# Performance work log

Measured on AMD Instinct MI355X. Metric: run time of the kernel, lower is better.

## Reference

```python
import jax, jax.numpy as jnp
import numpy as np

EMBED_DIM = 512
NUM_HEADS = 8
HEAD_DIM = EMBED_DIM // NUM_HEADS


def setup_inputs() -> dict:
    key = jax.random.key(0)
    ks = jax.random.split(key, 5)
    B, N, D = 2, 4096, EMBED_DIM
    s_in = 1.0 / np.sqrt(D)
    x = jax.random.normal(ks[0], (B, N, D), dtype=jnp.float32)
    qkv_w = jax.random.uniform(ks[1], (3 * D, D), dtype=jnp.float32, minval=-s_in, maxval=s_in)
    qkv_b = jax.random.uniform(ks[2], (3 * D,), dtype=jnp.float32, minval=-s_in, maxval=s_in)
    out_w = jax.random.uniform(ks[3], (D, D), dtype=jnp.float32, minval=-s_in, maxval=s_in)
    out_b = jax.random.uniform(ks[4], (D,), dtype=jnp.float32, minval=-s_in, maxval=s_in)
    return {"x": x, "qkv_w": qkv_w, "qkv_b": qkv_b, "out_w": out_w, "out_b": out_b}


def reference(x, qkv_w, qkv_b, out_w, out_b):
    B, N, D = x.shape
    H, Hd = NUM_HEADS, HEAD_DIM
    # qkv projection: [B,N,3D] -> [3,B,H,N,Hd]
    qkv = x @ qkv_w.T + qkv_b
    qkv = qkv.reshape(B, N, 3, H, Hd).transpose(2, 0, 3, 1, 4)
    q, k, v = qkv[0], qkv[1], qkv[2]
    scale = 1.0 / jnp.sqrt(jnp.asarray(Hd, dtype=x.dtype))
    scores = jnp.einsum("bhnd,bhmd->bhnm", q, k) * scale  # [B,H,N,N]
    weights = jax.nn.softmax(scores, axis=-1)
    out = jnp.einsum("bhnm,bhmd->bhnd", weights, v)  # [B,H,N,Hd]
    out = out.transpose(0, 2, 1, 3).reshape(B, N, D)
    return out @ out_w.T + out_b
```

## Files before the change

kernel.cpp:

```cpp
#include <hip/hip_runtime.h>

typedef __attribute__((ext_vector_type(8))) short short8;
typedef __attribute__((ext_vector_type(2))) float f32x2;
typedef __attribute__((ext_vector_type(4))) float f32x4;
typedef __attribute__((ext_vector_type(16))) float f32x16;
typedef unsigned short u16;
typedef unsigned int u32;

#define SCQ 0.18033688011112042f

__device__ __forceinline__ u16 f2b(float f) {
  unsigned u = __builtin_bit_cast(unsigned, f);
  u += 0x7FFFu + ((u >> 16) & 1u);
  return (u16)(u >> 16);
}

__device__ __forceinline__ u32 cvtpk(float a, float b) {
  u32 r;
  asm("v_cvt_pk_bf16_f32 %0, %1, %2" : "=v"(r) : "v"(a), "v"(b));
  return r;
}

__device__ __forceinline__ float ex2(float x) { return __builtin_amdgcn_exp2f(x); }

__device__ __forceinline__ void gl_lds16(const u16* g, u16* l) {
  __builtin_amdgcn_global_load_lds(
      (const __attribute__((address_space(1))) unsigned int*)g,
      (__attribute__((address_space(3))) unsigned int*)l, 16, 0, 0);
}

__global__ __launch_bounds__(256) void convert_k(
    const float* __restrict__ x, const float* __restrict__ w1, const float* __restrict__ w2,
    u16* __restrict__ xb, u16* __restrict__ w1b, u16* __restrict__ w2b) {
  const int NXv = (8192 * 512) / 4;
  const int NW1v = (1536 * 512) / 4;
  const int NW2v = (512 * 512) / 4;
  int i = blockIdx.x * 256 + threadIdx.x;
  const float4* src;
  u16* dst;
  int j;
  float scale = 1.0f;
  if (i < NXv) {
    src = (const float4*)x; dst = xb; j = i;
  } else if (i < NXv + NW1v) {
    j = i - NXv; src = (const float4*)w1; dst = w1b;
    if (j < (512 * 512) / 4) scale = SCQ;
  } else {
    j = i - NXv - NW1v;
    if (j >= NW2v) return;
    src = (const float4*)w2; dst = w2b;
  }
  float4 v = src[j];
  ushort4 o;
  o.x = f2b(v.x * scale); o.y = f2b(v.y * scale);
  o.z = f2b(v.z * scale); o.w = f2b(v.w * scale);
  *reinterpret_cast<ushort4*>(dst + (size_t)j * 4) = o;
}

__global__ __launch_bounds__(256) void qkv_gemm(
    const u16* __restrict__ Ab, const u16* __restrict__ Bw, const float* __restrict__ bias,
    u16* __restrict__ Qd, u16* __restrict__ Kd, u16* __restrict__ Vtd) {
  const int m0 = blockIdx.x * 128, n0 = blockIdx.y * 128;
  const int tid = threadIdx.x, wave = tid >> 6, lane = tid & 63;
  const int g = lane >> 4, lr = lane & 15;
  const int wm = (wave >> 1) * 64, wn = (wave & 1) * 64;
  __shared__ alignas(16) u16 smem[32768];

  f32x4 acc[4][4];
#pragma unroll
  for (int mf = 0; mf < 4; ++mf)
#pragma unroll
    for (int nf = 0; nf < 4; ++nf)
#pragma unroll
      for (int r = 0; r < 4; ++r) acc[mf][nf][r] = 0.0f;

  const int gid0 = wave * 64 + lane;

#define QKV_STAGE(buf, k0)                                                         \
  {                                                                                \
    u16* Ad_ = smem + (buf) * 8192;                                                \
    u16* Bd_ = smem + 16384 + (buf) * 8192;                                        \
    _Pragma("unroll")                                                              \
    for (int c = 0; c < 4; ++c) {                                                  \
      const int gid = c * 256 + gid0;                                              \
      const int row = gid >> 3;                                                    \
      const int col = ((gid & 7) ^ (row & 7)) << 3;                                \
      gl_lds16(Ab + (size_t)(m0 + row) * 512 + (k0) + col,                         \
               Ad_ + (size_t)(c * 256 + wave * 64) * 8);                           \
      gl_lds16(Bw + (size_t)(n0 + row) * 512 + (k0) + col,                         \
               Bd_ + (size_t)(c * 256 + wave * 64) * 8);                           \
    }                                                                              \
  }

  QKV_STAGE(0, 0);
  __syncthreads();

#pragma unroll 1
  for (int kt = 0; kt < 8; ++kt) {
    const int cur = kt & 1;
    if (kt + 1 < 8) QKV_STAGE(cur ^ 1, (kt + 1) * 64);

    const u16* Ac = smem + cur * 8192;
    const u16* Bc = smem + 16384 + cur * 8192;
#pragma unroll
    for (int kb = 0; kb < 2; ++kb) {
      short8 bf[4], af[4];
#pragma unroll
      for (int nf = 0; nf < 4; ++nf)
        bf[nf] = *reinterpret_cast<const short8*>(
            &Bc[(wn + nf * 16 + lr) * 64 + (((kb * 4 + g) ^ (lr & 7)) << 3)]);
#pragma unroll
      for (int mf = 0; mf < 4; ++mf)
        af[mf] = *reinterpret_cast<const short8*>(
            &Ac[(wm + mf * 16 + lr) * 64 + (((kb * 4 + g) ^ (lr & 7)) << 3)]);
#pragma unroll
      for (int mf = 0; mf < 4; ++mf)
#pragma unroll
        for (int nf = 0; nf < 4; ++nf)
          acc[mf][nf] = __builtin_amdgcn_mfma_f32_16x16x32_bf16(af[mf], bf[nf], acc[mf][nf], 0, 0, 0);
    }
    __syncthreads();
  }
#undef QKV_STAGE

  u16* Ct = smem;
  const int b = m0 >> 12;
  const int which = n0 >> 9;
  const int nloc = m0 & 4095;

  if (which < 2) {
#pragma unroll
    for (int mf = 0; mf < 4; ++mf)
#pragma unroll
      for (int nf = 0; nf < 4; ++nf) {
        const int col_l = wn + nf * 16 + lr;
        float bv = bias[n0 + col_l];
        if (which == 0) bv *= SCQ;
#pragma unroll
        for (int r = 0; r < 4; ++r)
          Ct[(wm + mf * 16 + g * 4 + r) * 136 + col_l] = f2b(acc[mf][nf][r] + bv);
      }
    __syncthreads();
    u16* const dst0 = (which == 0) ? Qd : Kd;
#pragma unroll
    for (int p = 0; p < 8; ++p) {
      const int idx = p * 256 + tid;
      const int row = idx >> 4;
      const int c8 = (idx & 15) << 3;
      short8 v = *reinterpret_cast<const short8*>(&Ct[row * 136 + c8]);
      const int col = n0 + c8;
      const int h = (col & 511) >> 6, hd = col & 63;
      *reinterpret_cast<short8*>(
          dst0 + ((size_t)(b * 8 + h) * 4096 + nloc + row) * 64 + hd) = v;
    }
  } else {
#pragma unroll
    for (int mf = 0; mf < 4; ++mf)
#pragma unroll
      for (int nf = 0; nf < 4; ++nf) {
        const int col_l = wn + nf * 16 + lr;
        const float bv = bias[n0 + col_l];
        const int row0 = wm + mf * 16 + g * 4;
        ushort4 pk;
        pk.x = f2b(acc[mf][nf][0] + bv);
        pk.y = f2b(acc[mf][nf][1] + bv);
        pk.z = f2b(acc[mf][nf][2] + bv);
        pk.w = f2b(acc[mf][nf][3] + bv);
        *reinterpret_cast<ushort4*>(&Ct[col_l * 136 + row0]) = pk;
      }
    __syncthreads();
#pragma unroll
    for (int p = 0; p < 8; ++p) {
      const int idx = p * 256 + tid;
      const int col_l = idx >> 4;
      const int c8 = (idx & 15) << 3;
      short8 v = *reinterpret_cast<const short8*>(&Ct[col_l * 136 + c8]);
      const int col = n0 + col_l;
      const int h = (col & 511) >> 6, hd = col & 63;
      *reinterpret_cast<short8*>(
          Vtd + ((size_t)(b * 8 + h) * 64 + hd) * 4096 + nloc + c8) = v;
    }
  }
}

__global__ __launch_bounds__(256, 2) void attn13(
    const u16* __restrict__ Qd, const u16* __restrict__ Kd, const u16* __restrict__ Vtd,
    float* __restrict__ Op, float* __restrict__ Lp) {
  int f = blockIdx.x;
  int xcd = f & 7, slot = f >> 3;
  int bh = (xcd << 1) + (slot >> 5);
  int rem = slot & 31;
  int half = rem >> 4;
  int qb = rem & 15;

  const int tid = threadIdx.x, wave = tid >> 6, lane = tid & 63;
  const int hi = lane >> 5, lq = lane & 31;

  const u16* Qh = Qd + (size_t)bh * (4096 * 64);
  const u16* Kh = Kd + (size_t)bh * (4096 * 64);
  const u16* Vh = Vtd + (size_t)bh * (64 * 4096);
  float* Oh = Op + (size_t)half * (8192 * 512);
  float* Lh = Lp + (size_t)half * (16 * 4096);

  __shared__ alignas(16) u16 Kl[2][128 * 64];

  const int qrow_base = qb * 256 + wave * 64;

  short8 qf[2][4];
#pragma unroll
  for (int qt = 0; qt < 2; ++qt)
#pragma unroll
    for (int s = 0; s < 4; ++s)
      qf[qt][s] = *reinterpret_cast<const short8*>(
          Qh + (size_t)(qrow_base + qt * 32 + lq) * 64 + s * 16 + hi * 8);

  f32x16 acc[2][2];
#pragma unroll
  for (int qt = 0; qt < 2; ++qt)
#pragma unroll
    for (int dt = 0; dt < 2; ++dt)
#pragma unroll
      for (int i = 0; i < 16; ++i) acc[qt][dt][i] = 0.0f;

  f32x16 Z;
#pragma unroll
  for (int i = 0; i < 16; ++i) Z[i] = 0.0f;

  float lrun[2] = {0.0f, 0.0f};

  const int kv0 = half * 2048;
  const int gid0 = wave * 64 + lane;

#pragma unroll
  for (int c = 0; c < 4; ++c) {
    const int gid = c * 256 + gid0;
    const int row = gid >> 3;
    const int col = ((gid & 7) ^ (row & 7)) << 3;
    gl_lds16(Kh + (size_t)(kv0 + row) * 64 + col, &Kl[0][(c * 256 + wave * 64) * 8]);
  }
  __syncthreads();

  f32x16 stA0, stA1, stB0, stB1;
  short8 vfA[2][2], vfB[2][2];
  short8 pbA0[2], pbA1[2], pbB0[2], pbB1[2];

#define QK_HALF(st0, st1, h)                                                        \
  {                                                                                 \
    const int rb = ((h) * 32 + lq) * 64;                                            \
    __builtin_amdgcn_s_setprio(1);                                                  \
    _Pragma("unroll")                                                               \
    for (int s = 0; s < 4; ++s) {                                                   \
      const int ch = ((2 * s + hi) ^ (lq & 7)) << 3;                                \
      short8 kf = *reinterpret_cast<const short8*>(&Kl[cur][rb + ch]);              \
      if (s == 0) {                                                                 \
        st0 = __builtin_amdgcn_mfma_f32_32x32x16_bf16(kf, qf[0][0], Z, 0, 0, 0);    \
        st1 = __builtin_amdgcn_mfma_f32_32x32x16_bf16(kf, qf[1][0], Z, 0, 0, 0);    \
      } else {                                                                      \
        st0 = __builtin_amdgcn_mfma_f32_32x32x16_bf16(kf, qf[0][s], st0, 0, 0, 0);  \
        st1 = __builtin_amdgcn_mfma_f32_32x32x16_bf16(kf, qf[1][s], st1, 0, 0, 0);  \
      }                                                                             \
    }                                                                               \
    __builtin_amdgcn_s_setprio(0);                                                  \
  }

#define LOADV_HALF(vf, h)                                                           \
  {                                                                                 \
    const int off = kbase + (h) * 32 + hi * 8;                                      \
    vf[0][0] = *reinterpret_cast<const short8*>(Vh + (size_t)lq * 4096 + off);      \
    vf[0][1] = *reinterpret_cast<const short8*>(Vh + (size_t)(32 + lq) * 4096 + off); \
    vf[1][0] = *reinterpret_cast<const short8*>(Vh + (size_t)lq * 4096 + off + 16); \
    vf[1][1] = *reinterpret_cast<const short8*>(Vh + (size_t)(32 + lq) * 4096 + off + 16); \
  }

#define SM_QT(stq, pbq, qt_idx)                                                     \
  {                                                                                 \
    f32x2 p2[8];                                                                    \
    _Pragma("unroll")                                                               \
    for (int j = 0; j < 8; ++j) {                                                   \
      p2[j][0] = ex2(stq[2 * j]);                                                   \
      p2[j][1] = ex2(stq[2 * j + 1]);                                               \
    }                                                                               \
    f32x2 s0 = (p2[0] + p2[1]) + (p2[2] + p2[3]);                                   \
    f32x2 s1 = (p2[4] + p2[5]) + (p2[6] + p2[7]);                                   \
    f32x2 sm = s0 + s1;                                                             \
    lrun[qt_idx] += sm[0] + sm[1];                                                  \
    _Pragma("unroll")                                                               \
    for (int t = 0; t < 2; ++t) {                                                   \
      u32 wa = cvtpk(p2[4 * t + 0][0], p2[4 * t + 0][1]);                           \
      u32 wb = cvtpk(p2[4 * t + 2][0], p2[4 * t + 2][1]);                           \
      u32 wc = cvtpk(p2[4 * t + 1][0], p2[4 * t + 1][1]);                           \
      u32 wd = cvtpk(p2[4 * t + 3][0], p2[4 * t + 3][1]);                           \
      asm volatile("v_permlane32_swap_b32 %0, %1" : "+v"(wa), "+v"(wb));            \
      asm volatile("v_permlane32_swap_b32 %0, %1" : "+v"(wc), "+v"(wd));            \
      int4 wv;                                                                      \
      wv.x = (int)wa; wv.y = (int)wc; wv.z = (int)wb; wv.w = (int)wd;               \
      pbq[t] = __builtin_bit_cast(short8, wv);                                      \
    }                                                                               \
  }

#define PV_HALF(vf, pb0, pb1)                                                       \
  {                                                                                 \
    __builtin_amdgcn_s_setprio(1);                                                  \
    _Pragma("unroll")                                                               \
    for (int t = 0; t < 2; ++t) {                                                   \
      acc[0][0] = __builtin_amdgcn_mfma_f32_32x32x16_bf16(vf[t][0], pb0[t], acc[0][0], 0, 0, 0); \
      acc[0][1] = __builtin_amdgcn_mfma_f32_32x32x16_bf16(vf[t][1], pb0[t], acc[0][1], 0, 0, 0); \
      acc[1][0] = __builtin_amdgcn_mfma_f32_32x32x16_bf16(vf[t][0], pb1[t], acc[1][0], 0, 0, 0); \
      acc[1][1] = __builtin_amdgcn_mfma_f32_32x32x16_bf16(vf[t][1], pb1[t], acc[1][1], 0, 0, 0); \
    }                                                                               \
    __builtin_amdgcn_s_setprio(0);                                                  \
  }

#pragma unroll 1
  for (int kt = 0; kt < 16; ++kt) {
    const int cur = kt & 1;
    const int kbase = kv0 + kt * 128;

    if (kt + 1 < 16) {
      const u16* kn = Kh + (size_t)(kbase + 128) * 64;
#pragma unroll
      for (int c = 0; c < 4; ++c) {
        const int gid = c * 256 + gid0;
        const int row = gid >> 3;
        const int col = ((gid & 7) ^ (row & 7)) << 3;
        gl_lds16(kn + (size_t)row * 64 + col, &Kl[cur ^ 1][(c * 256 + wave * 64) * 8]);
      }
    }

    QK_HALF(stA0, stA1, 0);
    LOADV_HALF(vfA, 0);
#pragma unroll
    for (int hp = 0; hp < 2; ++hp) {
      const int h = hp * 2;
      QK_HALF(stB0, stB1, h + 1);
      LOADV_HALF(vfB, h + 1);
      SM_QT(stA0, pbA0, 0);
      SM_QT(stA1, pbA1, 1);
      PV_HALF(vfA, pbA0, pbA1);
      if (hp == 0) {
        QK_HALF(stA0, stA1, h + 2);
        LOADV_HALF(vfA, h + 2);
      }
      SM_QT(stB0, pbB0, 0);
      SM_QT(stB1, pbB1, 1);
      PV_HALF(vfB, pbB0, pbB1);
    }

    __syncthreads();
  }
#undef QK_HALF
#undef LOADV_HALF
#undef SM_QT
#undef PV_HALF

  const int b = bh >> 3, h = bh & 7;
#pragma unroll
  for (int qt = 0; qt < 2; ++qt) {
    const int qn = qrow_base + qt * 32 + lq;
    const size_t rowoff = ((size_t)(b * 4096 + qn)) * 512 + h * 64;
#pragma unroll
    for (int dt = 0; dt < 2; ++dt)
#pragma unroll
      for (int t = 0; t < 4; ++t) {
        f32x4 v4;
        v4[0] = acc[qt][dt][4 * t + 0];
        v4[1] = acc[qt][dt][4 * t + 1];
        v4[2] = acc[qt][dt][4 * t + 2];
        v4[3] = acc[qt][dt][4 * t + 3];
        *reinterpret_cast<f32x4*>(Oh + rowoff + dt * 32 + t * 8 + hi * 4) = v4;
      }
    float lt = lrun[qt] + __shfl_xor(lrun[qt], 32);
    if (hi == 0) Lh[(bh << 12) + qn] = lt;
  }
}

__global__ __launch_bounds__(256) void combine_k(
    const float* __restrict__ Op, const float* __restrict__ Lp,
    u16* __restrict__ attnb) {
  int idx = blockIdx.x * 256 + threadIdx.x;
  int row = idx >> 7, c4 = idx & 127;
  int b = row >> 12, n = row & 4095, h = c4 >> 4;
  int li = (((b << 3) + h) << 12) + n;
  float l = Lp[li] + Lp[li + 65536];
  float inv = 1.0f / l;
  const int STRIDE = 8192 * 512 / 4;
  float4 o0 = reinterpret_cast<const float4*>(Op)[idx];
  float4 o1 = reinterpret_cast<const float4*>(Op)[idx + STRIDE];
  ushort4 o;
  o.x = f2b((o0.x + o1.x) * inv);
  o.y = f2b((o0.y + o1.y) * inv);
  o.z = f2b((o0.z + o1.z) * inv);
  o.w = f2b((o0.w + o1.w) * inv);
  *reinterpret_cast<ushort4*>(attnb + (size_t)idx * 4) = o;
}

__global__ __launch_bounds__(256) void out_gemm(
    const u16* __restrict__ Ab, const u16* __restrict__ Bw, const float* __restrict__ bias,
    float* __restrict__ out) {
  const int m0 = blockIdx.x * 128, n0 = blockIdx.y * 128;
  const int tid = threadIdx.x, wave = tid >> 6, lane = tid & 63;
  const int g = lane >> 4, lr = lane & 15;
  const int wm = (wave >> 1) * 64, wn = (wave & 1) * 64;
  __shared__ alignas(16) u16 smem[32768];

  f32x4 acc[4][4];
#pragma unroll
  for (int mf = 0; mf < 4; ++mf)
#pragma unroll
    for (int nf = 0; nf < 4; ++nf)
#pragma unroll
      for (int r = 0; r < 4; ++r) acc[mf][nf][r] = 0.0f;

  const int gid0 = wave * 64 + lane;

#define OUT_STAGE(buf, k0)                                                         \
  {                                                                                \
    u16* Ad_ = smem + (buf) * 8192;                                                \
    u16* Bd_ = smem + 16384 + (buf) * 8192;                                        \
    _Pragma("unroll")                                                              \
    for (int c = 0; c < 4; ++c) {                                                  \
      const int gid = c * 256 + gid0;                                              \
      const int row = gid >> 3;                                                    \
      const int col = ((gid & 7) ^ (row & 7)) << 3;                                \
      gl_lds16(Ab + (size_t)(m0 + row) * 512 + (k0) + col,                         \
               Ad_ + (size_t)(c * 256 + wave * 64) * 8);                           \
      gl_lds16(Bw + (size_t)(n0 + row) * 512 + (k0) + col,                         \
               Bd_ + (size_t)(c * 256 + wave * 64) * 8);                           \
    }                                                                              \
  }

  OUT_STAGE(0, 0);
  __syncthreads();

#pragma unroll 1
  for (int kt = 0; kt < 8; ++kt) {
    const int cur = kt & 1;
    if (kt + 1 < 8) OUT_STAGE(cur ^ 1, (kt + 1) * 64);

    const u16* Ac = smem + cur * 8192;
    const u16* Bc = smem + 16384 + cur * 8192;
#pragma unroll
    for (int kb = 0; kb < 2; ++kb) {
      short8 bf[4], af[4];
#pragma unroll
      for (int nf = 0; nf < 4; ++nf)
        bf[nf] = *reinterpret_cast<const short8*>(
            &Bc[(wn + nf * 16 + lr) * 64 + (((kb * 4 + g) ^ (lr & 7)) << 3)]);
#pragma unroll
      for (int mf = 0; mf < 4; ++mf)
        af[mf] = *reinterpret_cast<const short8*>(
            &Ac[(wm + mf * 16 + lr) * 64 + (((kb * 4 + g) ^ (lr & 7)) << 3)]);
#pragma unroll
      for (int mf = 0; mf < 4; ++mf)
#pragma unroll
        for (int nf = 0; nf < 4; ++nf)
          acc[mf][nf] = __builtin_amdgcn_mfma_f32_16x16x32_bf16(af[mf], bf[nf], acc[mf][nf], 0, 0, 0);
    }
    __syncthreads();
  }
#undef OUT_STAGE

#pragma unroll
  for (int mf = 0; mf < 4; ++mf)
#pragma unroll
    for (int nf = 0; nf < 4; ++nf)
#pragma unroll
      for (int r = 0; r < 4; ++r) {
        int row = m0 + wm + mf * 16 + g * 4 + r;
        int col = n0 + wn + nf * 16 + lr;
        out[(size_t)row * 512 + col] = acc[mf][nf][r] + bias[col];
      }
}

extern "C" void kernel_launch(void* const* d_in, const int* in_sizes, int n_in,
                              void* d_out, int out_size, void* d_ws, size_t ws_size,
                              hipStream_t stream) {
  const float* x = (const float*)d_in[0];
  const float* qkv_w = (const float*)d_in[1];
  const float* qkv_b = (const float*)d_in[2];
  const float* out_w = (const float*)d_in[3];
  const float* out_b = (const float*)d_in[4];
  float* out = (float*)d_out;

  char* ws = (char*)d_ws;
  u16* xb    = (u16*)(ws + 0);
  u16* w1b   = (u16*)(ws + 8388608);
  u16* w2b   = (u16*)(ws + 9961472);
  u16* Qd    = (u16*)(ws + 10485760);
  u16* Kd    = (u16*)(ws + 18874368);
  u16* Vtd   = (u16*)(ws + 27262976);
  u16* attnb = (u16*)(ws + 35651584);
  float* Op  = (float*)(ws + 44040192);
  float* Lp  = (float*)(ws + 77594624);

  convert_k<<<5120, 256, 0, stream>>>(x, qkv_w, out_w, xb, w1b, w2b);
  qkv_gemm<<<dim3(64, 12), 256, 0, stream>>>(xb, w1b, qkv_b, Qd, Kd, Vtd);
  attn13<<<512, 256, 0, stream>>>(Qd, Kd, Vtd, Op, Lp);
  combine_k<<<4096, 256, 0, stream>>>(Op, Lp, attnb);
  out_gemm<<<dim3(64, 4), 256, 0, stream>>>(attnb, w2b, out_b, out);
}
```

Before: 131.4 us.

## Halve per-wave query tile in attention to double block count and occupancy

The attention kernel now gives each wave 32 query rows instead of 64, so a block covers 128 queries and the grid doubles to 1024 blocks, with launch bounds raised to 3 blocks per CU. Fewer accumulator and score registers per wave should allow more concurrent waves and better latency hiding on the 256 CUs. In exchange, each K tile loaded into LDS and each V fragment read from global is reused by half as many queries, which doubles K/V traffic and LDS fill work per unit of compute.

```diff
diff --git a/kernel.cpp b/kernel.cpp
--- a/kernel.cpp
+++ b/kernel.cpp
@@ -183,15 +183,15 @@
   }
 }
 
-__global__ __launch_bounds__(256, 2) void attn13(
+__global__ __launch_bounds__(256, 3) void attn20(
     const u16* __restrict__ Qd, const u16* __restrict__ Kd, const u16* __restrict__ Vtd,
     float* __restrict__ Op, float* __restrict__ Lp) {
   int f = blockIdx.x;
   int xcd = f & 7, slot = f >> 3;
-  int bh = (xcd << 1) + (slot >> 5);
-  int rem = slot & 31;
-  int half = rem >> 4;
-  int qb = rem & 15;
+  int bh = (xcd << 1) + (slot >> 6);
+  int rem = slot & 63;
+  int half = rem >> 5;
+  int qb = rem & 31;
 
   const int tid = threadIdx.x, wave = tid >> 6, lane = tid & 63;
   const int hi = lane >> 5, lq = lane & 31;
@@ -204,29 +204,25 @@
 
   __shared__ alignas(16) u16 Kl[2][128 * 64];
 
-  const int qrow_base = qb * 256 + wave * 64;
-
-  short8 qf[2][4];
-#pragma unroll
-  for (int qt = 0; qt < 2; ++qt)
-#pragma unroll
-    for (int s = 0; s < 4; ++s)
-      qf[qt][s] = *reinterpret_cast<const short8*>(
-          Qh + (size_t)(qrow_base + qt * 32 + lq) * 64 + s * 16 + hi * 8);
-
-  f32x16 acc[2][2];
-#pragma unroll
-  for (int qt = 0; qt < 2; ++qt)
-#pragma unroll
-    for (int dt = 0; dt < 2; ++dt)
-#pragma unroll
-      for (int i = 0; i < 16; ++i) acc[qt][dt][i] = 0.0f;
+  const int qrow = qb * 128 + wave * 32;
+
+  short8 qf[4];
+#pragma unroll
+  for (int s = 0; s < 4; ++s)
+    qf[s] = *reinterpret_cast<const short8*>(
+        Qh + (size_t)(qrow + lq) * 64 + s * 16 + hi * 8);
+
+  f32x16 acc[2];
+#pragma unroll
+  for (int dt = 0; dt < 2; ++dt)
+#pragma unroll
+    for (int i = 0; i < 16; ++i) acc[dt][i] = 0.0f;
 
   f32x16 Z;
 #pragma unroll
   for (int i = 0; i < 16; ++i) Z[i] = 0.0f;
 
-  float lrun[2] = {0.0f, 0.0f};
+  float lrun = 0.0f;
 
   const int kv0 = half * 2048;
   const int gid0 = wave * 64 + lane;
@@ -240,11 +236,11 @@
   }
   __syncthreads();
 
-  f32x16 stA0, stA1, stB0, stB1;
+  f32x16 stA, stB;
   short8 vfA[2][2], vfB[2][2];
-  short8 pbA0[2], pbA1[2], pbB0[2], pbB1[2];
-
-#define QK_HALF(st0, st1, h)                                                        \
+  short8 pbA[2], pbB[2];
+
+#define QK_HALF(st0, h)                                                             \
   {                                                                                 \
     const int rb = ((h) * 32 + lq) * 64;                                            \
     __builtin_amdgcn_s_setprio(1);                                                  \
@@ -252,13 +248,8 @@
     for (int s = 0; s < 4; ++s) {                                                   \
       const int ch = ((2 * s + hi) ^ (lq & 7)) << 3;                                \
       short8 kf = *reinterpret_cast<const short8*>(&Kl[cur][rb + ch]);              \
-      if (s == 0) {                                                                 \
-        st0 = __builtin_amdgcn_mfma_f32_32x32x16_bf16(kf, qf[0][0], Z, 0, 0, 0);    \
-        st1 = __builtin_amdgcn_mfma_f32_32x32x16_bf16(kf, qf[1][0], Z, 0, 0, 0);    \
-      } else {                                                                      \
-        st0 = __builtin_amdgcn_mfma_f32_32x32x16_bf16(kf, qf[0][s], st0, 0, 0, 0);  \
-        st1 = __builtin_amdgcn_mfma_f32_32x32x16_bf16(kf, qf[1][s], st1, 0, 0, 0);  \
-      }                                                                             \
+      if (s == 0) st0 = __builtin_amdgcn_mfma_f32_32x32x16_bf16(kf, qf[0], Z, 0, 0, 0); \
+      else        st0 = __builtin_amdgcn_mfma_f32_32x32x16_bf16(kf, qf[s], st0, 0, 0, 0); \
     }                                                                               \
     __builtin_amdgcn_s_setprio(0);                                                  \
   }
@@ -272,7 +263,7 @@
     vf[1][1] = *reinterpret_cast<const short8*>(Vh + (size_t)(32 + lq) * 4096 + off + 16); \
   }
 
-#define SM_QT(stq, pbq, qt_idx)                                                     \
+#define SM_HALF(stq, pbq)                                                           \
   {                                                                                 \
     f32x2 p2[8];                                                                    \
     _Pragma("unroll")                                                               \
@@ -283,7 +274,7 @@
     f32x2 s0 = (p2[0] + p2[1]) + (p2[2] + p2[3]);                                   \
     f32x2 s1 = (p2[4] + p2[5]) + (p2[6] + p2[7]);                                   \
     f32x2 sm = s0 + s1;                                                             \
-    lrun[qt_idx] += sm[0] + sm[1];                                                  \
+    lrun += sm[0] + sm[1];                                                          \
     _Pragma("unroll")                                                               \
     for (int t = 0; t < 2; ++t) {                                                   \
       u32 wa = cvtpk(p2[4 * t + 0][0], p2[4 * t + 0][1]);                           \
@@ -298,15 +289,13 @@
     }                                                                               \
   }
 
-#define PV_HALF(vf, pb0, pb1)                                                       \
+#define PV_HALF(vf, pb)                                                             \
   {                                                                                 \
     __builtin_amdgcn_s_setprio(1);                                                  \
     _Pragma("unroll")                                                               \
     for (int t = 0; t < 2; ++t) {                                                   \
-      acc[0][0] = __builtin_amdgcn_mfma_f32_32x32x16_bf16(vf[t][0], pb0[t], acc[0][0], 0, 0, 0); \
-      acc[0][1] = __builtin_amdgcn_mfma_f32_32x32x16_bf16(vf[t][1], pb0[t], acc[0][1], 0, 0, 0); \
-      acc[1][0] = __builtin_amdgcn_mfma_f32_32x32x16_bf16(vf[t][0], pb1[t], acc[1][0], 0, 0, 0); \
-      acc[1][1] = __builtin_amdgcn_mfma_f32_32x32x16_bf16(vf[t][1], pb1[t], acc[1][1], 0, 0, 0); \
+      acc[0] = __builtin_amdgcn_mfma_f32_32x32x16_bf16(vf[t][0], pb[t], acc[0], 0, 0, 0); \
+      acc[1] = __builtin_amdgcn_mfma_f32_32x32x16_bf16(vf[t][1], pb[t], acc[1], 0, 0, 0); \
     }                                                                               \
     __builtin_amdgcn_s_setprio(0);                                                  \
   }
@@ -327,49 +316,46 @@
       }
     }
 
-    QK_HALF(stA0, stA1, 0);
+    QK_HALF(stA, 0);
     LOADV_HALF(vfA, 0);
 #pragma unroll
     for (int hp = 0; hp < 2; ++hp) {
       const int h = hp * 2;
-      QK_HALF(stB0, stB1, h + 1);
+      QK_HALF(stB, h + 1);
       LOADV_HALF(vfB, h + 1);
-      SM_QT(stA0, pbA0, 0);
-      SM_QT(stA1, pbA1, 1);
-      PV_HALF(vfA, pbA0, pbA1);
+      SM_HALF(stA, pbA);
+      PV_HALF(vfA, pbA);
       if (hp == 0) {
-        QK_HALF(stA0, stA1, h + 2);
+        QK_HALF(stA, h + 2);
         LOADV_HALF(vfA, h + 2);
       }
-      SM_QT(stB0, pbB0, 0);
-      SM_QT(stB1, pbB1, 1);
-      PV_HALF(vfB, pbB0, pbB1);
+      SM_HALF(stB, pbB);
+      PV_HALF(vfB, pbB);
     }
 
     __syncthreads();
   }
 #undef QK_HALF
 #undef LOADV_HALF
-#undef SM_QT
+#undef SM_HALF
 #undef PV_HALF
 
   const int b = bh >> 3, h = bh & 7;
-#pragma unroll
-  for (int qt = 0; qt < 2; ++qt) {
-    const int qn = qrow_base + qt * 32 + lq;
+  {
+    const int qn = qrow + lq;
     const size_t rowoff = ((size_t)(b * 4096 + qn)) * 512 + h * 64;
 #pragma unroll
     for (int dt = 0; dt < 2; ++dt)
 #pragma unroll
       for (int t = 0; t < 4; ++t) {
         f32x4 v4;
-        v4[0] = acc[qt][dt][4 * t + 0];
-        v4[1] = acc[qt][dt][4 * t + 1];
-        v4[2] = acc[qt][dt][4 * t + 2];
-        v4[3] = acc[qt][dt][4 * t + 3];
+        v4[0] = acc[dt][4 * t + 0];
+        v4[1] = acc[dt][4 * t + 1];
+        v4[2] = acc[dt][4 * t + 2];
+        v4[3] = acc[dt][4 * t + 3];
         *reinterpret_cast<f32x4*>(Oh + rowoff + dt * 32 + t * 8 + hi * 4) = v4;
       }
-    float lt = lrun[qt] + __shfl_xor(lrun[qt], 32);
+    float lt = lrun + __shfl_xor(lrun, 32);
     if (hi == 0) Lh[(bh << 12) + qn] = lt;
   }
 }
@@ -495,7 +481,7 @@
 
   convert_k<<<5120, 256, 0, stream>>>(x, qkv_w, out_w, xb, w1b, w2b);
   qkv_gemm<<<dim3(64, 12), 256, 0, stream>>>(xb, w1b, qkv_b, Qd, Kd, Vtd);
-  attn13<<<512, 256, 0, stream>>>(Qd, Kd, Vtd, Op, Lp);
+  attn20<<<1024, 256, 0, stream>>>(Qd, Kd, Vtd, Op, Lp);
   combine_k<<<4096, 256, 0, stream>>>(Op, Lp, attnb);
   out_gemm<<<dim3(64, 4), 256, 0, stream>>>(attnb, w2b, out_b, out);
 }
```

New measurement: 181.6 us. 38.2% more time.
